# Kernel tuning notes

Hardware: AMD Instinct MI355X
Metric: run time of the kernel (lower is better)

## Reference

```python
import jax, jax.numpy as jnp
import numpy as np

EPS = 1e-6
CHUNK = 64
GATE_LOGIT_NORMALIZER = 16.0
NUM_HEADS = 4


def _rms(x, w):
    return x * jax.lax.rsqrt(jnp.mean(x * x, axis=-1, keepdims=True) + EPS) * w


def _gla_chunk(q, k, v, glog, num_heads):
    # q,k: [B,T,Dk] v: [B,T,Dv] glog: [B,T,Dk] (log decay, <=0)
    B, T, Dk = q.shape
    Dv = v.shape[-1]
    dk, dv = Dk // num_heads, Dv // num_heads
    Nc = T // CHUNK

    def split(x, d):
        # [B,T,H*d] -> [B,H,Nc,C,d]
        return x.reshape(B, T, num_heads, d).transpose(0, 2, 1, 3).reshape(B, num_heads, Nc, CHUNK, d)

    q, k, v, g = split(q, dk), split(k, dk), split(v, dv), split(glog, dk)
    b = jnp.cumsum(g, axis=3)  # inclusive cumulative log-decay within chunk
    scale = dk ** -0.5
    qe = q * jnp.exp(b) * scale

    # intra-chunk: A[t,s] = sum_d q_t k_s exp(b_t - b_s), causal (t>=s)
    mask = jnp.tril(jnp.ones((CHUNK, CHUNK), dtype=bool))
    A = jnp.einsum('bhncd,bhnsd->bhncs', qe, k * jnp.exp(-b))
    A = jnp.where(mask, A, 0.0)
    o_intra = jnp.einsum('bhncs,bhnsd->bhncd', A, v)

    # inter-chunk recurrence over state S: [B,H,dk,dv]
    def step(S, xs):
        qe_c, k_c, v_c, b_c = xs  # [B,H,C,*]
        blast = b_c[:, :, -1, :]                      # [B,H,dk]
        o_inter = jnp.einsum('bhcd,bhde->bhce', qe_c, S)
        kd = k_c * jnp.exp(blast[:, :, None, :] - b_c)
        S_new = S * jnp.exp(blast)[..., None] + jnp.einsum('bhcd,bhce->bhde', kd, v_c)
        return S_new, o_inter

    S0 = jnp.zeros((B, num_heads, dk, dv), q.dtype)
    xs = tuple(jnp.moveaxis(t, 2, 0) for t in (qe, k, v, b))
    _, o_inter = jax.lax.scan(step, S0, xs)
    o = o_intra + jnp.moveaxis(o_inter, 0, 2)  # [B,H,Nc,C,dv]
    return o.reshape(B, num_heads, T, dv).transpose(0, 2, 1, 3)  # [B,T,H,dv]


def setup_inputs() -> dict:
    key = jax.random.key(0)
    ks = jax.random.split(key, 12)
    B, T, Hs = 4, 2048, 1024
    Dk, Dv, I, R = 512, 1024, 2816, 16
    p = lambda k, s: jax.random.normal(k, s, jnp.float32) * 0.02
    return {
        'hidden_states': jax.random.normal(ks[0], (B, T, Hs), jnp.float32),
        'attn_norm_w': jnp.ones((Hs,), jnp.float32),
        'Wq': p(ks[1], (Hs, Dk)), 'Wk': p(ks[2], (Hs, Dk)), 'Wv': p(ks[3], (Hs, Dv)),
        'Wg': p(ks[4], (Hs, Dv)),
        'Wgk1': p(ks[5], (Hs, R)), 'Wgk2': p(ks[6], (R, Dk)), 'bgk2': jnp.zeros((Dk,), jnp.float32),
        'gnorm_w': jnp.ones((Dv // NUM_HEADS,), jnp.float32),
        'Wo': p(ks[7], (Dv, Hs)),
        'mlp_norm_w': jnp.ones((Hs,), jnp.float32),
        'W_gate': p(ks[8], (Hs, I)), 'W_up': p(ks[9], (Hs, I)), 'W_down': p(ks[10], (I, Hs)),
    }


def reference(hidden_states, attn_norm_w, Wq, Wk, Wv, Wg, Wgk1, Wgk2, bgk2,
              gnorm_w, Wo, mlp_norm_w, W_gate, W_up, W_down):
    x = hidden_states
    h = _rms(x, attn_norm_w)
    q, k, v = h @ Wq, h @ Wk, h @ Wv
    glog = jax.nn.log_sigmoid(h @ Wgk1 @ Wgk2 + bgk2) / GATE_LOGIT_NORMALIZER
    o = _gla_chunk(q, k, v, glog, NUM_HEADS)          # [B,T,H,dv]
    g_out = (h @ Wg).reshape(o.shape)
    o = _rms(o, gnorm_w) * (g_out * jax.nn.sigmoid(g_out))  # per-head RMSNorm + swish gate
    attn_out = o.reshape(x.shape[0], x.shape[1], -1) @ Wo
    # fused residual RMSNorm
    x2 = attn_out + x
    n = _rms(x2, mlp_norm_w)
    mlp = (jax.nn.silu(n @ W_gate) * (n @ W_up)) @ W_down
    return x2 + mlp
```

## Files before the change

### kernel.cpp

```cpp
#include <hip/hip_runtime.h>

typedef unsigned short u16;
typedef __attribute__((ext_vector_type(8))) short bf8_t;
typedef __attribute__((ext_vector_type(4))) float f4_t;

#define MFMA_B16(a,b,c) __builtin_amdgcn_mfma_f32_16x16x32_bf16(a,b,c,0,0,0)

__device__ __forceinline__ u16 f2bf(float f){
  union{ float f; unsigned u; } x; x.f = f;
  unsigned r = x.u + 0x7FFFu + ((x.u >> 16) & 1u);
  return (u16)(r >> 16);
}
__device__ __forceinline__ float bf2f(u16 u){
  union{ unsigned u; float f; } x; x.u = ((unsigned)u) << 16; return x.f;
}
__device__ __forceinline__ void gl_lds16(const void* g, void* l){
  __builtin_amdgcn_global_load_lds(
      (const __attribute__((address_space(1))) unsigned int*)g,
      (__attribute__((address_space(3))) unsigned int*)l, 16, 0, 0);
}
__device__ __forceinline__ int swz128(int row, int cb){ return row*128 + (cb ^ ((row & 7)  << 4)); }
__device__ __forceinline__ int swz256(int row, int cb){ return row*256 + (cb ^ ((row & 15) << 4)); }

__device__ __forceinline__ void xcd_map(int gx, int gy, int& bm, int& bn){
  const int i   = blockIdx.y*gx + blockIdx.x;
  const int cpx = (gx*gy) >> 3;
  const int j   = (i & 7)*cpx + (i >> 3);
  const int k   = j / (gx*8);
  const int jl  = j - k*(gx*8);
  bn = jl >> 3;
  bm = k*8 + (jl & 7);
}

#define TOKS 8192
#define HS   1024
#define DKTOT 512
#define DVTOT 1024
#define IM   2816

__global__ __launch_bounds__(256) void k_transpose(
    const float* __restrict__ W, u16* __restrict__ Wt, int K, int N)
{
  __shared__ float tile[64][65];
  const int n0 = blockIdx.x*64, k0 = blockIdx.y*64;
  const int tx = threadIdx.x & 63, tg = threadIdx.x >> 6;
  #pragma unroll
  for(int i=0;i<16;i++){
    int kr = tg*16 + i;
    tile[kr][tx] = W[(size_t)(k0+kr)*N + n0 + tx];
  }
  __syncthreads();
  #pragma unroll
  for(int i=0;i<16;i++){
    int nr = tg*16 + i;
    Wt[(size_t)(n0+nr)*K + k0 + tx] = f2bf(tile[tx][nr]);
  }
}

__global__ __launch_bounds__(256) void k_rmsnorm(
    const float* __restrict__ X, const float* __restrict__ W, u16* __restrict__ H)
{
  __shared__ float red[4];
  const size_t row = blockIdx.x;
  const int t = threadIdx.x;
  const float4 v = ((const float4*)(X + row*1024))[t];
  float ss = v.x*v.x + v.y*v.y + v.z*v.z + v.w*v.w;
  #pragma unroll
  for(int m=32;m>=1;m>>=1) ss += __shfl_xor(ss, m, 64);
  if((t & 63) == 0) red[t >> 6] = ss;
  __syncthreads();
  ss = red[0] + red[1] + red[2] + red[3];
  const float rs = rsqrtf(ss*(1.f/1024.f) + 1e-6f);
  const float4 w = ((const float4*)W)[t];
  ushort4 o;
  o.x = f2bf(v.x*rs*w.x);
  o.y = f2bf(v.y*rs*w.y);
  o.z = f2bf(v.z*rs*w.z);
  o.w = f2bf(v.w*rs*w.w);
  ((ushort4*)H)[row*256 + t] = o;
}

__global__ __launch_bounds__(256) void k_glog(
    const u16* __restrict__ H, const float* __restrict__ W1,
    const float* __restrict__ W2, const float* __restrict__ bias,
    float* __restrict__ G)
{
  __shared__ float hs[1024];
  __shared__ float red[16][17];
  __shared__ float rr[16];
  const size_t row = blockIdx.x;
  const int t = threadIdx.x;
  #pragma unroll
  for(int j=0;j<4;j++) hs[t*4+j] = bf2f(H[row*1024 + t*4 + j]);
  __syncthreads();
  const int r = t & 15, c = t >> 4;
  float acc = 0.f;
  #pragma unroll
  for(int j=0;j<64;j++){
    int k = c*64 + ((j + c) & 63);
    acc += hs[k] * W1[(size_t)k*16 + r];
  }
  red[c][r] = acc;
  __syncthreads();
  if(t < 16){
    float s2 = 0.f;
    #pragma unroll
    for(int cc=0;cc<16;cc++) s2 += red[cc][t];
    rr[t] = s2;
  }
  __syncthreads();
  #pragma unroll
  for(int dd=0;dd<2;dd++){
    int dcol = t + dd*256;
    float z = bias[dcol];
    #pragma unroll
    for(int j=0;j<16;j++) z += rr[j]*W2[j*512 + dcol];
    float ls = fminf(z, 0.f) - log1pf(__expf(-fabsf(z)));
    G[row*512 + dcol] = ls * 0.0625f;
  }
}

enum { E_BF16=1, E_ADDF32=2, E_SILUMUL=3, E_TRANS=4 };

template<int EPI>
__global__ __launch_bounds__(512, 2) void k_gemm8(
    const u16* __restrict__ A, const u16* __restrict__ Bt,
    void* __restrict__ Cp, const void* __restrict__ aux,
    int M, int N, int K)
{
  __shared__ __align__(16) u16 lds[3*24576];
  const int t = threadIdx.x;
  const int wv = t >> 6, ln = t & 63, lr = ln & 15, lg = ln >> 4;
  const int wm = wv >> 2, wn = wv & 3;
  int bm, bn; xcd_map(gridDim.x, gridDim.y, bm, bn);
  const int m0 = bm*128, n0 = bn*256;
  const int NT = K >> 6;

  const int sr = t >> 3;
  const int sc = ((t & 7)*16 ^ ((sr & 7) << 4)) >> 1;
  const u16* Asrc = A  + (size_t)(m0 + sr)*K + sc;
  const u16* Bsrc = Bt + (size_t)(n0 + sr)*K + sc;

  auto stage = [&](int T){
    const int b = T % 3;
    const size_t ko = (size_t)T * 64;
    u16* dA = lds + b*24576 + wv*512;
    u16* dB = lds + b*24576 + 8192 + wv*512;
    gl_lds16(Asrc + ko,                    dA);
    gl_lds16(Asrc + (size_t)64*K + ko,     dA + 4096);
    #pragma unroll
    for(int j=0;j<4;j++)
      gl_lds16(Bsrc + (size_t)(j*64)*K + ko, dB + j*4096);
  };

  f4_t acc[4][4];
  #pragma unroll
  for(int i=0;i<4;i++)
    #pragma unroll
    for(int j=0;j<4;j++) acc[i][j] = f4_t{0.f,0.f,0.f,0.f};

  const int rA = wm*64 + lr;
  const int rB = wn*64 + lr;
  const int cxor = (lr & 7) << 4;

  auto compute = [&](int b){
    const char* La = (const char*)(lds + b*24576);
    const char* Lb = La + 16384;
    #pragma unroll
    for(int kk=0;kk<2;++kk){
      const int cb = (kk*64 + lg*16) ^ cxor;
      bf8_t af[4], bfr[4];
      #pragma unroll
      for(int m=0;m<4;m++) af[m]  = *(const bf8_t*)(La + (rA + m*16)*128 + cb);
      #pragma unroll
      for(int n=0;n<4;n++) bfr[n] = *(const bf8_t*)(Lb + (rB + n*16)*128 + cb);
      __builtin_amdgcn_s_setprio(1);
      #pragma unroll
      for(int m=0;m<4;m++)
        #pragma unroll
        for(int n=0;n<4;n++)
          acc[m][n] = MFMA_B16(af[m], bfr[n], acc[m][n]);
      __builtin_amdgcn_s_setprio(0);
    }
  };

  stage(0);
  stage(1);

  for(int T=0; T<NT-1; ++T){
    asm volatile("s_waitcnt vmcnt(6)" ::: "memory");
    __builtin_amdgcn_s_barrier();
    asm volatile("" ::: "memory");
    __builtin_amdgcn_sched_barrier(0);
    if(T+2 < NT) stage(T+2);
    compute(T % 3);
  }
  asm volatile("s_waitcnt vmcnt(0)" ::: "memory");
  __builtin_amdgcn_s_barrier();
  asm volatile("" ::: "memory");
  __builtin_amdgcn_sched_barrier(0);
  compute((NT-1) % 3);

  #pragma unroll
  for(int m=0;m<4;m++){
    #pragma unroll
    for(int n=0;n<4;n++){
      const int row0 = m0 + wm*64 + m*16 + lg*4;
      const int col  = n0 + wn*64 + n*16 + lr;
      if constexpr(EPI==E_TRANS){
        ushort4 u;
        u.x = f2bf(acc[m][n][0]); u.y = f2bf(acc[m][n][1]);
        u.z = f2bf(acc[m][n][2]); u.w = f2bf(acc[m][n][3]);
        *(ushort4*)((u16*)Cp + (size_t)col*M + row0) = u;
      } else {
        #pragma unroll
        for(int r=0;r<4;r++){
          const size_t idx = (size_t)(row0+r)*N + col;
          float v = acc[m][n][r];
          if constexpr(EPI==E_BF16) ((u16*)Cp)[idx] = f2bf(v);
          else if constexpr(EPI==E_ADDF32) ((float*)Cp)[idx] = v + ((const float*)aux)[idx];
          else if constexpr(EPI==E_SILUMUL){
            float u = bf2f(((const u16*)aux)[idx]);
            ((u16*)Cp)[idx] = f2bf(u * v / (1.f + __expf(-v)));
          }
        }
      }
    }
  }
}

__global__ __launch_bounds__(256) void k_gla_a(
    const u16* __restrict__ QK,
    const u16* __restrict__ VT, const float* __restrict__ G,
    u16* __restrict__ QE, u16* __restrict__ OI,
    u16* __restrict__ CT, float* __restrict__ DEC)
{
  __shared__ __align__(16) u16 qe_s[64*128];
  __shared__ __align__(16) u16 ke_s[64*128];
  __shared__ __align__(16) u16 kd_s[128*64];
  __shared__ __align__(16) u16 a_s [64*64];

  const int bid = blockIdx.x;
  const int nc = bid & 31, hh = (bid >> 5) & 3, bb = bid >> 7;
  const int bh = bb*4 + hh;
  const int tok0 = bb*2048 + nc*64;
  const int t = threadIdx.x;
  const size_t cbase = (size_t)(bh*32 + nc);

  if(t < 128){
    const int d = t;
    const int col = hh*128 + d;
    float g[64];
    float blast = 0.f;
    #pragma unroll
    for(int i=0;i<64;i++){
      g[i] = G[(size_t)(tok0+i)*512 + col];
      blast += g[i];
    }
    DEC[cbase*128 + d] = __expf(blast);
    float cum = 0.f;
    #pragma unroll
    for(int i=0;i<64;i++){
      cum += g[i];
      float qv = bf2f(QK[(size_t)(tok0+i)*1024 + col]);
      float kv = bf2f(QK[(size_t)(tok0+i)*1024 + 512 + col]);
      float qe = qv * __expf(cum) * 0.08838834764831845f;
      float ke = kv * __expf(-cum);
      float kd = kv * __expf(blast - cum);
      *(u16*)((char*)qe_s + swz256(i, d*2)) = f2bf(qe);
      *(u16*)((char*)ke_s + swz256(i, d*2)) = f2bf(ke);
      *(u16*)((char*)kd_s + swz128(d, i*2)) = f2bf(kd);
      QE[(cbase*64 + i)*128 + d] = f2bf(qe);
    }
  }
  __syncthreads();

  const int wv = t >> 6, ln = t & 63, lr = ln & 15, lg = ln >> 4;

  bf8_t aq[4];
  #pragma unroll
  for(int ks=0;ks<4;ks++)
    aq[ks] = *(const bf8_t*)((const char*)qe_s + swz256(wv*16 + lr, ks*64 + lg*16));
  #pragma unroll
  for(int n=0;n<4;n++){
    f4_t accA = f4_t{0.f,0.f,0.f,0.f};
    #pragma unroll
    for(int ks=0;ks<4;ks++){
      bf8_t bk = *(const bf8_t*)((const char*)ke_s + swz256(n*16 + lr, ks*64 + lg*16));
      accA = MFMA_B16(aq[ks], bk, accA);
    }
    #pragma unroll
    for(int r=0;r<4;r++){
      int i = wv*16 + lg*4 + r;
      int s = n*16 + lr;
      float v = (s <= i) ? accA[r] : 0.f;
      *(u16*)((char*)a_s + swz128(i, s*2)) = f2bf(v);
    }
  }
  __syncthreads();

  bf8_t af[2], kf[2][2];
  #pragma unroll
  for(int ks=0;ks<2;ks++)
    af[ks] = *(const bf8_t*)((const char*)a_s + swz128(wv*16 + lr, ks*64 + lg*16));
  #pragma unroll
  for(int p=0;p<2;p++)
    #pragma unroll
    for(int ks=0;ks<2;ks++)
      kf[p][ks] = *(const bf8_t*)((const char*)kd_s + swz128((2*wv+p)*16 + lr, ks*64 + lg*16));

  #pragma unroll 4
  for(int ne=0; ne<16; ne++){
    bf8_t vf[2];
    #pragma unroll
    for(int ks=0;ks<2;ks++)
      vf[ks] = *(const bf8_t*)(VT + (size_t)(hh*256 + ne*16 + lr)*8192 + tok0 + ks*32 + lg*8);
    f4_t ao = f4_t{0.f,0.f,0.f,0.f};
    ao = MFMA_B16(af[0], vf[0], ao);
    ao = MFMA_B16(af[1], vf[1], ao);
    #pragma unroll
    for(int r=0;r<4;r++)
      OI[(cbase*64 + wv*16 + lg*4 + r)*256 + ne*16 + lr] = f2bf(ao[r]);
    f4_t c0 = f4_t{0.f,0.f,0.f,0.f}, c1 = f4_t{0.f,0.f,0.f,0.f};
    c0 = MFMA_B16(kf[0][0], vf[0], c0);
    c0 = MFMA_B16(kf[0][1], vf[1], c0);
    c1 = MFMA_B16(kf[1][0], vf[0], c1);
    c1 = MFMA_B16(kf[1][1], vf[1], c1);
    u16* dst = CT + (cbase*256 + ne*16 + lr)*128;
    ushort4 u0, u1;
    u0.x=f2bf(c0[0]); u0.y=f2bf(c0[1]); u0.z=f2bf(c0[2]); u0.w=f2bf(c0[3]);
    u1.x=f2bf(c1[0]); u1.y=f2bf(c1[1]); u1.z=f2bf(c1[2]); u1.w=f2bf(c1[3]);
    *(ushort4*)(dst + (2*wv+0)*16 + lg*4) = u0;
    *(ushort4*)(dst + (2*wv+1)*16 + lg*4) = u1;
  }
}

__global__ __launch_bounds__(256) void k_scan(
    u16* __restrict__ CTST, const float* __restrict__ DEC)
{
  const int idx = blockIdx.x*256 + threadIdx.x;
  const int d = idx & 127;
  const int e = (idx >> 7) & 255;
  const int bh = idx >> 15;
  float s = 0.f;
  for(int n=0;n<32;n++){
    const size_t off = ((size_t)(bh*32 + n)*256 + e)*128 + d;
    float c = bf2f(CTST[off]);
    CTST[off] = f2bf(s);
    s = s * DEC[(bh*32+n)*128 + d] + c;
  }
}

__global__ __launch_bounds__(256) void k_gla_c(
    const u16* __restrict__ QE, const u16* __restrict__ ST,
    const u16* __restrict__ OI, const u16* __restrict__ GO,
    const float* __restrict__ GW, u16* __restrict__ OG)
{
  const int bid = blockIdx.x;
  const int nc = bid & 31, hh = (bid >> 5) & 3, bb = bid >> 7;
  const int bh = bb*4 + hh;
  const int tok0 = bb*2048 + nc*64;
  const int t = threadIdx.x;
  const int wv = t >> 6, ln = t & 63, lr = ln & 15, lg = ln >> 4;
  const size_t cbase = (size_t)(bh*32 + nc);

  bf8_t qf[4];
  #pragma unroll
  for(int ks=0;ks<4;ks++)
    qf[ks] = *(const bf8_t*)(QE + (cbase*64 + wv*16 + lr)*128 + ks*32 + lg*8);

  f4_t acc[16];
  #pragma unroll
  for(int ne=0;ne<16;ne++){
    f4_t a = f4_t{0.f,0.f,0.f,0.f};
    #pragma unroll
    for(int ks=0;ks<4;ks++){
      bf8_t sf = *(const bf8_t*)(ST + (cbase*256 + ne*16 + lr)*128 + ks*32 + lg*8);
      a = MFMA_B16(qf[ks], sf, a);
    }
    acc[ne] = a;
  }

  float vals[16][4];
  float ss[4] = {0.f,0.f,0.f,0.f};
  #pragma unroll
  for(int ne=0;ne<16;ne++)
    #pragma unroll
    for(int r=0;r<4;r++){
      float v = acc[ne][r] + bf2f(OI[(cbase*64 + wv*16 + lg*4 + r)*256 + ne*16 + lr]);
      vals[ne][r] = v;
      ss[r] += v*v;
    }
  #pragma unroll
  for(int r=0;r<4;r++){
    ss[r] += __shfl_xor(ss[r], 1, 64);
    ss[r] += __shfl_xor(ss[r], 2, 64);
    ss[r] += __shfl_xor(ss[r], 4, 64);
    ss[r] += __shfl_xor(ss[r], 8, 64);
  }
  float rs[4];
  #pragma unroll
  for(int r=0;r<4;r++) rs[r] = rsqrtf(ss[r]*(1.f/256.f) + 1e-6f);

  #pragma unroll
  for(int ne=0;ne<16;ne++)
    #pragma unroll
    for(int r=0;r<4;r++){
      int i = wv*16 + lg*4 + r;
      int e = ne*16 + lr;
      const size_t idx = (size_t)(tok0+i)*1024 + hh*256 + e;
      float gg = bf2f(GO[idx]);
      float sg = gg / (1.f + __expf(-gg));
      OG[idx] = f2bf(vals[ne][r]*rs[r]*GW[e]*sg);
    }
}

constexpr size_t OFF_WQT    = 0;
constexpr size_t OFF_WKT    = OFF_WQT    + (size_t)DKTOT*HS*2;
constexpr size_t OFF_WVT    = OFF_WKT    + (size_t)DKTOT*HS*2;
constexpr size_t OFF_WGT    = OFF_WVT    + (size_t)DVTOT*HS*2;
constexpr size_t OFF_WOT    = OFF_WGT    + (size_t)DVTOT*HS*2;
constexpr size_t OFF_WGATET = OFF_WOT    + (size_t)HS*DVTOT*2;
constexpr size_t OFF_WUPT   = OFF_WGATET + (size_t)IM*HS*2;
constexpr size_t OFF_WDOWNT = OFF_WUPT   + (size_t)IM*HS*2;
constexpr size_t OFF_QE     = OFF_WDOWNT + (size_t)HS*IM*2;
constexpr size_t OFF_CTST   = OFF_QE     + (size_t)TOKS*DKTOT*2;
constexpr size_t OFF_DEC    = OFF_CTST   + (size_t)512*256*128*2;
constexpr size_t OFF_R1     = OFF_DEC    + (size_t)512*128*4;
constexpr size_t OFF_QKB    = OFF_R1;
constexpr size_t OFF_GLOG   = OFF_QKB    + (size_t)TOKS*1024*2;
constexpr size_t OFF_VT     = OFF_GLOG   + (size_t)TOKS*DKTOT*4;
constexpr size_t OFF_UP     = OFF_R1;
constexpr size_t OFF_R3     = OFF_R1 + 50331648;
constexpr size_t OFF_H      = OFF_R3;
constexpr size_t OFF_OI     = OFF_R3;
constexpr size_t OFF_N2     = OFF_R3;
constexpr size_t OFF_R4     = OFF_R3 + 16777216;
constexpr size_t OFF_GO     = OFF_R4;
constexpr size_t OFF_OG     = OFF_R4;
constexpr size_t WS_NEED    = OFF_R4 + 16777216;

extern "C" void kernel_launch(void* const* d_in, const int* in_sizes, int n_in,
                              void* d_out, int out_size, void* d_ws, size_t ws_size,
                              hipStream_t stream) {
  (void)in_sizes; (void)n_in; (void)out_size;
  if (ws_size < WS_NEED) return;

  const float* x       = (const float*)d_in[0];
  const float* attn_w  = (const float*)d_in[1];
  const float* Wq      = (const float*)d_in[2];
  const float* Wk      = (const float*)d_in[3];
  const float* Wv      = (const float*)d_in[4];
  const float* Wg      = (const float*)d_in[5];
  const float* Wgk1    = (const float*)d_in[6];
  const float* Wgk2    = (const float*)d_in[7];
  const float* bgk2    = (const float*)d_in[8];
  const float* gnw     = (const float*)d_in[9];
  const float* Wo      = (const float*)d_in[10];
  const float* mlpw    = (const float*)d_in[11];
  const float* Wgate   = (const float*)d_in[12];
  const float* Wup     = (const float*)d_in[13];
  const float* Wdown   = (const float*)d_in[14];
  char* ws = (char*)d_ws;

  u16*   wqt   = (u16*)(ws + OFF_WQT);
  u16*   wkt   = (u16*)(ws + OFF_WKT);
  u16*   wvt   = (u16*)(ws + OFF_WVT);
  u16*   wgt   = (u16*)(ws + OFF_WGT);
  u16*   wot   = (u16*)(ws + OFF_WOT);
  u16*   wgatet= (u16*)(ws + OFF_WGATET);
  u16*   wupt  = (u16*)(ws + OFF_WUPT);
  u16*   wdownt= (u16*)(ws + OFF_WDOWNT);
  u16*   qeb   = (u16*)(ws + OFF_QE);
  u16*   ctst  = (u16*)(ws + OFF_CTST);
  float* decb  = (float*)(ws + OFF_DEC);
  u16*   qkb   = (u16*)(ws + OFF_QKB);
  float* glogb = (float*)(ws + OFF_GLOG);
  u16*   vtb   = (u16*)(ws + OFF_VT);
  u16*   upb   = (u16*)(ws + OFF_UP);
  u16*   hb    = (u16*)(ws + OFF_H);
  u16*   oib   = (u16*)(ws + OFF_OI);
  u16*   n2b   = (u16*)(ws + OFF_N2);
  u16*   gob   = (u16*)(ws + OFF_GO);
  u16*   ogb   = (u16*)(ws + OFF_OG);
  float* x2b   = (float*)d_out;

  dim3 blk(256);
  dim3 blk8(512);

  k_transpose<<<dim3(DKTOT/64, HS/64), blk, 0, stream>>>(Wq, wqt, HS, DKTOT);
  k_transpose<<<dim3(DKTOT/64, HS/64), blk, 0, stream>>>(Wk, wkt, HS, DKTOT);
  k_transpose<<<dim3(DVTOT/64, HS/64), blk, 0, stream>>>(Wv, wvt, HS, DVTOT);
  k_transpose<<<dim3(DVTOT/64, HS/64), blk, 0, stream>>>(Wg, wgt, HS, DVTOT);
  k_transpose<<<dim3(HS/64, DVTOT/64), blk, 0, stream>>>(Wo, wot, DVTOT, HS);
  k_transpose<<<dim3(IM/64, HS/64), blk, 0, stream>>>(Wgate, wgatet, HS, IM);
  k_transpose<<<dim3(IM/64, HS/64), blk, 0, stream>>>(Wup, wupt, HS, IM);
  k_transpose<<<dim3(HS/64, IM/64), blk, 0, stream>>>(Wdown, wdownt, IM, HS);

  k_rmsnorm<<<TOKS, blk, 0, stream>>>(x, attn_w, hb);
  k_gemm8<E_BF16> <<<dim3(4, 64), blk8, 0, stream>>>(hb, wqt, qkb, nullptr, TOKS, 1024, HS);
  k_gemm8<E_TRANS><<<dim3(4, 64), blk8, 0, stream>>>(hb, wvt, vtb, nullptr, TOKS, DVTOT, HS);
  k_gemm8<E_BF16> <<<dim3(4, 64), blk8, 0, stream>>>(hb, wgt, gob, nullptr, TOKS, DVTOT, HS);
  k_glog<<<TOKS, blk, 0, stream>>>(hb, Wgk1, Wgk2, bgk2, glogb);

  k_gla_a<<<512, blk, 0, stream>>>(qkb, vtb, glogb, qeb, oib, ctst, decb);
  k_scan <<<2048, blk, 0, stream>>>(ctst, decb);
  k_gla_c<<<512, blk, 0, stream>>>(qeb, ctst, oib, gob, gnw, ogb);

  k_gemm8<E_ADDF32><<<dim3(4, 64), blk8, 0, stream>>>(ogb, wot, x2b, x, TOKS, HS, DVTOT);

  k_rmsnorm<<<TOKS, blk, 0, stream>>>(x2b, mlpw, n2b);
  k_gemm8<E_BF16>   <<<dim3(11, 64), blk8, 0, stream>>>(n2b, wupt,   upb, nullptr, TOKS, IM, HS);
  k_gemm8<E_SILUMUL><<<dim3(11, 64), blk8, 0, stream>>>(n2b, wgatet, upb, upb,     TOKS, IM, HS);
  k_gemm8<E_ADDF32> <<<dim3(4, 64),  blk8, 0, stream>>>(upb, wdownt, x2b, x2b,     TOKS, HS, IM);
}
```

Measured before the change: 438.6 us.

## Merge weight transposes, fuse QKV/G projections into one GEMM, split cumsum

Collapses the eight per-weight transpose launches into a single segmented kernel, and replaces the three separate projection GEMMs (QK, V-transposed, G) with one wide GEMM over a contiguous transposed-weight buffer, using a new epilogue that routes columns to the right destination. The GLA chunk-prep stage now uses all 256 threads, split into two token halves combined through shared-memory partial sums, instead of leaving half the block idle. These changes are meant to cut launch overhead and improve GPU fill for the small GEMMs. They depend on the weight buffers being laid out contiguously and on the new epilogue's routing being correct.

After: 418.4 us. -4.6%, faster.

```diff
diff --git a/kernel.cpp b/kernel.cpp
--- a/kernel.cpp
+++ b/kernel.cpp
@@ -5,415 +5,12 @@
 typedef __attribute__((ext_vector_type(4))) float f4_t;
 
 #define MFMA_B16(a,b,c) __builtin_amdgcn_mfma_f32_16x16x32_bf16(a,b,c,0,0,0)
-
-__device__ __forceinline__ u16 f2bf(float f){
-  union{ float f; unsigned u; } x; x.f = f;
-  unsigned r = x.u + 0x7FFFu + ((x.u >> 16) & 1u);
-  return (u16)(r >> 16);
-}
-__device__ __forceinline__ float bf2f(u16 u){
-  union{ unsigned u; float f; } x; x.u = ((unsigned)u) << 16; return x.f;
-}
-__device__ __forceinline__ void gl_lds16(const void* g, void* l){
-  __builtin_amdgcn_global_load_lds(
-      (const __attribute__((address_space(1))) unsigned int*)g,
-      (__attribute__((address_space(3))) unsigned int*)l, 16, 0, 0);
-}
-__device__ __forceinline__ int swz128(int row, int cb){ return row*128 + (cb ^ ((row & 7)  << 4)); }
-__device__ __forceinline__ int swz256(int row, int cb){ return row*256 + (cb ^ ((row & 15) << 4)); }
-
-__device__ __forceinline__ void xcd_map(int gx, int gy, int& bm, int& bn){
-  const int i   = blockIdx.y*gx + blockIdx.x;
-  const int cpx = (gx*gy) >> 3;
-  const int j   = (i & 7)*cpx + (i >> 3);
-  const int k   = j / (gx*8);
-  const int jl  = j - k*(gx*8);
-  bn = jl >> 3;
-  bm = k*8 + (jl & 7);
-}
 
 #define TOKS 8192
 #define HS   1024
 #define DKTOT 512
 #define DVTOT 1024
 #define IM   2816
-
-__global__ __launch_bounds__(256) void k_transpose(
-    const float* __restrict__ W, u16* __restrict__ Wt, int K, int N)
-{
-  __shared__ float tile[64][65];
-  const int n0 = blockIdx.x*64, k0 = blockIdx.y*64;
-  const int tx = threadIdx.x & 63, tg = threadIdx.x >> 6;
-  #pragma unroll
-  for(int i=0;i<16;i++){
-    int kr = tg*16 + i;
-    tile[kr][tx] = W[(size_t)(k0+kr)*N + n0 + tx];
-  }
-  __syncthreads();
-  #pragma unroll
-  for(int i=0;i<16;i++){
-    int nr = tg*16 + i;
-    Wt[(size_t)(n0+nr)*K + k0 + tx] = f2bf(tile[tx][nr]);
-  }
-}
-
-__global__ __launch_bounds__(256) void k_rmsnorm(
-    const float* __restrict__ X, const float* __restrict__ W, u16* __restrict__ H)
-{
-  __shared__ float red[4];
-  const size_t row = blockIdx.x;
-  const int t = threadIdx.x;
-  const float4 v = ((const float4*)(X + row*1024))[t];
-  float ss = v.x*v.x + v.y*v.y + v.z*v.z + v.w*v.w;
-  #pragma unroll
-  for(int m=32;m>=1;m>>=1) ss += __shfl_xor(ss, m, 64);
-  if((t & 63) == 0) red[t >> 6] = ss;
-  __syncthreads();
-  ss = red[0] + red[1] + red[2] + red[3];
-  const float rs = rsqrtf(ss*(1.f/1024.f) + 1e-6f);
-  const float4 w = ((const float4*)W)[t];
-  ushort4 o;
-  o.x = f2bf(v.x*rs*w.x);
-  o.y = f2bf(v.y*rs*w.y);
-  o.z = f2bf(v.z*rs*w.z);
-  o.w = f2bf(v.w*rs*w.w);
-  ((ushort4*)H)[row*256 + t] = o;
-}
-
-__global__ __launch_bounds__(256) void k_glog(
-    const u16* __restrict__ H, const float* __restrict__ W1,
-    const float* __restrict__ W2, const float* __restrict__ bias,
-    float* __restrict__ G)
-{
-  __shared__ float hs[1024];
-  __shared__ float red[16][17];
-  __shared__ float rr[16];
-  const size_t row = blockIdx.x;
-  const int t = threadIdx.x;
-  #pragma unroll
-  for(int j=0;j<4;j++) hs[t*4+j] = bf2f(H[row*1024 + t*4 + j]);
-  __syncthreads();
-  const int r = t & 15, c = t >> 4;
-  float acc = 0.f;
-  #pragma unroll
-  for(int j=0;j<64;j++){
-    int k = c*64 + ((j + c) & 63);
-    acc += hs[k] * W1[(size_t)k*16 + r];
-  }
-  red[c][r] = acc;
-  __syncthreads();
-  if(t < 16){
-    float s2 = 0.f;
-    #pragma unroll
-    for(int cc=0;cc<16;cc++) s2 += red[cc][t];
-    rr[t] = s2;
-  }
-  __syncthreads();
-  #pragma unroll
-  for(int dd=0;dd<2;dd++){
-    int dcol = t + dd*256;
-    float z = bias[dcol];
-    #pragma unroll
-    for(int j=0;j<16;j++) z += rr[j]*W2[j*512 + dcol];
-    float ls = fminf(z, 0.f) - log1pf(__expf(-fabsf(z)));
-    G[row*512 + dcol] = ls * 0.0625f;
-  }
-}
-
-enum { E_BF16=1, E_ADDF32=2, E_SILUMUL=3, E_TRANS=4 };
-
-template<int EPI>
-__global__ __launch_bounds__(512, 2) void k_gemm8(
-    const u16* __restrict__ A, const u16* __restrict__ Bt,
-    void* __restrict__ Cp, const void* __restrict__ aux,
-    int M, int N, int K)
-{
-  __shared__ __align__(16) u16 lds[3*24576];
-  const int t = threadIdx.x;
-  const int wv = t >> 6, ln = t & 63, lr = ln & 15, lg = ln >> 4;
-  const int wm = wv >> 2, wn = wv & 3;
-  int bm, bn; xcd_map(gridDim.x, gridDim.y, bm, bn);
-  const int m0 = bm*128, n0 = bn*256;
-  const int NT = K >> 6;
-
-  const int sr = t >> 3;
-  const int sc = ((t & 7)*16 ^ ((sr & 7) << 4)) >> 1;
-  const u16* Asrc = A  + (size_t)(m0 + sr)*K + sc;
-  const u16* Bsrc = Bt + (size_t)(n0 + sr)*K + sc;
-
-  auto stage = [&](int T){
-    const int b = T % 3;
-    const size_t ko = (size_t)T * 64;
-    u16* dA = lds + b*24576 + wv*512;
-    u16* dB = lds + b*24576 + 8192 + wv*512;
-    gl_lds16(Asrc + ko,                    dA);
-    gl_lds16(Asrc + (size_t)64*K + ko,     dA + 4096);
-    #pragma unroll
-    for(int j=0;j<4;j++)
-      gl_lds16(Bsrc + (size_t)(j*64)*K + ko, dB + j*4096);
-  };
-
-  f4_t acc[4][4];
-  #pragma unroll
-  for(int i=0;i<4;i++)
-    #pragma unroll
-    for(int j=0;j<4;j++) acc[i][j] = f4_t{0.f,0.f,0.f,0.f};
-
-  const int rA = wm*64 + lr;
-  const int rB = wn*64 + lr;
-  const int cxor = (lr & 7) << 4;
-
-  auto compute = [&](int b){
-    const char* La = (const char*)(lds + b*24576);
-    const char* Lb = La + 16384;
-    #pragma unroll
-    for(int kk=0;kk<2;++kk){
-      const int cb = (kk*64 + lg*16) ^ cxor;
-      bf8_t af[4], bfr[4];
-      #pragma unroll
-      for(int m=0;m<4;m++) af[m]  = *(const bf8_t*)(La + (rA + m*16)*128 + cb);
-      #pragma unroll
-      for(int n=0;n<4;n++) bfr[n] = *(const bf8_t*)(Lb + (rB + n*16)*128 + cb);
-      __builtin_amdgcn_s_setprio(1);
-      #pragma unroll
-      for(int m=0;m<4;m++)
-        #pragma unroll
-        for(int n=0;n<4;n++)
-          acc[m][n] = MFMA_B16(af[m], bfr[n], acc[m][n]);
-      __builtin_amdgcn_s_setprio(0);
-    }
-  };
-
-  stage(0);
-  stage(1);
-
-  for(int T=0; T<NT-1; ++T){
-    asm volatile("s_waitcnt vmcnt(6)" ::: "memory");
-    __builtin_amdgcn_s_barrier();
-    asm volatile("" ::: "memory");
-    __builtin_amdgcn_sched_barrier(0);
-    if(T+2 < NT) stage(T+2);
-    compute(T % 3);
-  }
-  asm volatile("s_waitcnt vmcnt(0)" ::: "memory");
-  __builtin_amdgcn_s_barrier();
-  asm volatile("" ::: "memory");
-  __builtin_amdgcn_sched_barrier(0);
-  compute((NT-1) % 3);
-
-  #pragma unroll
-  for(int m=0;m<4;m++){
-    #pragma unroll
-    for(int n=0;n<4;n++){
-      const int row0 = m0 + wm*64 + m*16 + lg*4;
-      const int col  = n0 + wn*64 + n*16 + lr;
-      if constexpr(EPI==E_TRANS){
-        ushort4 u;
-        u.x = f2bf(acc[m][n][0]); u.y = f2bf(acc[m][n][1]);
-        u.z = f2bf(acc[m][n][2]); u.w = f2bf(acc[m][n][3]);
-        *(ushort4*)((u16*)Cp + (size_t)col*M + row0) = u;
-      } else {
-        #pragma unroll
-        for(int r=0;r<4;r++){
-          const size_t idx = (size_t)(row0+r)*N + col;
-          float v = acc[m][n][r];
-          if constexpr(EPI==E_BF16) ((u16*)Cp)[idx] = f2bf(v);
-          else if constexpr(EPI==E_ADDF32) ((float*)Cp)[idx] = v + ((const float*)aux)[idx];
-          else if constexpr(EPI==E_SILUMUL){
-            float u = bf2f(((const u16*)aux)[idx]);
-            ((u16*)Cp)[idx] = f2bf(u * v / (1.f + __expf(-v)));
-          }
-        }
-      }
-    }
-  }
-}
-
-__global__ __launch_bounds__(256) void k_gla_a(
-    const u16* __restrict__ QK,
-    const u16* __restrict__ VT, const float* __restrict__ G,
-    u16* __restrict__ QE, u16* __restrict__ OI,
-    u16* __restrict__ CT, float* __restrict__ DEC)
-{
-  __shared__ __align__(16) u16 qe_s[64*128];
-  __shared__ __align__(16) u16 ke_s[64*128];
-  __shared__ __align__(16) u16 kd_s[128*64];
-  __shared__ __align__(16) u16 a_s [64*64];
-
-  const int bid = blockIdx.x;
-  const int nc = bid & 31, hh = (bid >> 5) & 3, bb = bid >> 7;
-  const int bh = bb*4 + hh;
-  const int tok0 = bb*2048 + nc*64;
-  const int t = threadIdx.x;
-  const size_t cbase = (size_t)(bh*32 + nc);
-
-  if(t < 128){
-    const int d = t;
-    const int col = hh*128 + d;
-    float g[64];
-    float blast = 0.f;
-    #pragma unroll
-    for(int i=0;i<64;i++){
-      g[i] = G[(size_t)(tok0+i)*512 + col];
-      blast += g[i];
-    }
-    DEC[cbase*128 + d] = __expf(blast);
-    float cum = 0.f;
-    #pragma unroll
-    for(int i=0;i<64;i++){
-      cum += g[i];
-      float qv = bf2f(QK[(size_t)(tok0+i)*1024 + col]);
-      float kv = bf2f(QK[(size_t)(tok0+i)*1024 + 512 + col]);
-      float qe = qv * __expf(cum) * 0.08838834764831845f;
-      float ke = kv * __expf(-cum);
-      float kd = kv * __expf(blast - cum);
-      *(u16*)((char*)qe_s + swz256(i, d*2)) = f2bf(qe);
-      *(u16*)((char*)ke_s + swz256(i, d*2)) = f2bf(ke);
-      *(u16*)((char*)kd_s + swz128(d, i*2)) = f2bf(kd);
-      QE[(cbase*64 + i)*128 + d] = f2bf(qe);
-    }
-  }
-  __syncthreads();
-
-  const int wv = t >> 6, ln = t & 63, lr = ln & 15, lg = ln >> 4;
-
-  bf8_t aq[4];
-  #pragma unroll
-  for(int ks=0;ks<4;ks++)
-    aq[ks] = *(const bf8_t*)((const char*)qe_s + swz256(wv*16 + lr, ks*64 + lg*16));
-  #pragma unroll
-  for(int n=0;n<4;n++){
-    f4_t accA = f4_t{0.f,0.f,0.f,0.f};
-    #pragma unroll
-    for(int ks=0;ks<4;ks++){
-      bf8_t bk = *(const bf8_t*)((const char*)ke_s + swz256(n*16 + lr, ks*64 + lg*16));
-      accA = MFMA_B16(aq[ks], bk, accA);
-    }
-    #pragma unroll
-    for(int r=0;r<4;r++){
-      int i = wv*16 + lg*4 + r;
-      int s = n*16 + lr;
-      float v = (s <= i) ? accA[r] : 0.f;
-      *(u16*)((char*)a_s + swz128(i, s*2)) = f2bf(v);
-    }
-  }
-  __syncthreads();
-
-  bf8_t af[2], kf[2][2];
-  #pragma unroll
-  for(int ks=0;ks<2;ks++)
-    af[ks] = *(const bf8_t*)((const char*)a_s + swz128(wv*16 + lr, ks*64 + lg*16));
-  #pragma unroll
-  for(int p=0;p<2;p++)
-    #pragma unroll
-    for(int ks=0;ks<2;ks++)
-      kf[p][ks] = *(const bf8_t*)((const char*)kd_s + swz128((2*wv+p)*16 + lr, ks*64 + lg*16));
-
-  #pragma unroll 4
-  for(int ne=0; ne<16; ne++){
-    bf8_t vf[2];
-    #pragma unroll
-    for(int ks=0;ks<2;ks++)
-      vf[ks] = *(const bf8_t*)(VT + (size_t)(hh*256 + ne*16 + lr)*8192 + tok0 + ks*32 + lg*8);
-    f4_t ao = f4_t{0.f,0.f,0.f,0.f};
-    ao = MFMA_B16(af[0], vf[0], ao);
-    ao = MFMA_B16(af[1], vf[1], ao);
-    #pragma unroll
-    for(int r=0;r<4;r++)
-      OI[(cbase*64 + wv*16 + lg*4 + r)*256 + ne*16 + lr] = f2bf(ao[r]);
-    f4_t c0 = f4_t{0.f,0.f,0.f,0.f}, c1 = f4_t{0.f,0.f,0.f,0.f};
-    c0 = MFMA_B16(kf[0][0], vf[0], c0);
-    c0 = MFMA_B16(kf[0][1], vf[1], c0);
-    c1 = MFMA_B16(kf[1][0], vf[0], c1);
-    c1 = MFMA_B16(kf[1][1], vf[1], c1);
-    u16* dst = CT + (cbase*256 + ne*16 + lr)*128;
-    ushort4 u0, u1;
-    u0.x=f2bf(c0[0]); u0.y=f2bf(c0[1]); u0.z=f2bf(c0[2]); u0.w=f2bf(c0[3]);
-    u1.x=f2bf(c1[0]); u1.y=f2bf(c1[1]); u1.z=f2bf(c1[2]); u1.w=f2bf(c1[3]);
-    *(ushort4*)(dst + (2*wv+0)*16 + lg*4) = u0;
-    *(ushort4*)(dst + (2*wv+1)*16 + lg*4) = u1;
-  }
-}
-
-__global__ __launch_bounds__(256) void k_scan(
-    u16* __restrict__ CTST, const float* __restrict__ DEC)
-{
-  const int idx = blockIdx.x*256 + threadIdx.x;
-  const int d = idx & 127;
-  const int e = (idx >> 7) & 255;
-  const int bh = idx >> 15;
-  float s = 0.f;
-  for(int n=0;n<32;n++){
-    const size_t off = ((size_t)(bh*32 + n)*256 + e)*128 + d;
-    float c = bf2f(CTST[off]);
-    CTST[off] = f2bf(s);
-    s = s * DEC[(bh*32+n)*128 + d] + c;
-  }
-}
-
-__global__ __launch_bounds__(256) void k_gla_c(
-    const u16* __restrict__ QE, const u16* __restrict__ ST,
-    const u16* __restrict__ OI, const u16* __restrict__ GO,
-    const float* __restrict__ GW, u16* __restrict__ OG)
-{
-  const int bid = blockIdx.x;
-  const int nc = bid & 31, hh = (bid >> 5) & 3, bb = bid >> 7;
-  const int bh = bb*4 + hh;
-  const int tok0 = bb*2048 + nc*64;
-  const int t = threadIdx.x;
-  const int wv = t >> 6, ln = t & 63, lr = ln & 15, lg = ln >> 4;
-  const size_t cbase = (size_t)(bh*32 + nc);
-
-  bf8_t qf[4];
-  #pragma unroll
-  for(int ks=0;ks<4;ks++)
-    qf[ks] = *(const bf8_t*)(QE + (cbase*64 + wv*16 + lr)*128 + ks*32 + lg*8);
-
-  f4_t acc[16];
-  #pragma unroll
-  for(int ne=0;ne<16;ne++){
-    f4_t a = f4_t{0.f,0.f,0.f,0.f};
-    #pragma unroll
-    for(int ks=0;ks<4;ks++){
-      bf8_t sf = *(const bf8_t*)(ST + (cbase*256 + ne*16 + lr)*128 + ks*32 + lg*8);
-      a = MFMA_B16(qf[ks], sf, a);
-    }
-    acc[ne] = a;
-  }
-
-  float vals[16][4];
-  float ss[4] = {0.f,0.f,0.f,0.f};
-  #pragma unroll
-  for(int ne=0;ne<16;ne++)
-    #pragma unroll
-    for(int r=0;r<4;r++){
-      float v = acc[ne][r] + bf2f(OI[(cbase*64 + wv*16 + lg*4 + r)*256 + ne*16 + lr]);
-      vals[ne][r] = v;
-      ss[r] += v*v;
-    }
-  #pragma unroll
-  for(int r=0;r<4;r++){
-    ss[r] += __shfl_xor(ss[r], 1, 64);
-    ss[r] += __shfl_xor(ss[r], 2, 64);
-    ss[r] += __shfl_xor(ss[r], 4, 64);
-    ss[r] += __shfl_xor(ss[r], 8, 64);
-  }
-  float rs[4];
-  #pragma unroll
-  for(int r=0;r<4;r++) rs[r] = rsqrtf(ss[r]*(1.f/256.f) + 1e-6f);
-
-  #pragma unroll
-  for(int ne=0;ne<16;ne++)
-    #pragma unroll
-    for(int r=0;r<4;r++){
-      int i = wv*16 + lg*4 + r;
-      int e = ne*16 + lr;
-      const size_t idx = (size_t)(tok0+i)*1024 + hh*256 + e;
-      float gg = bf2f(GO[idx]);
-      float sg = gg / (1.f + __expf(-gg));
-      OG[idx] = f2bf(vals[ne][r]*rs[r]*GW[e]*sg);
-    }
-}
 
 constexpr size_t OFF_WQT    = 0;
 constexpr size_t OFF_WKT    = OFF_WQT    + (size_t)DKTOT*HS*2;
@@ -440,6 +37,452 @@
 constexpr size_t OFF_OG     = OFF_R4;
 constexpr size_t WS_NEED    = OFF_R4 + 16777216;
 
+__device__ __forceinline__ u16 f2bf(float f){
+  union{ float f; unsigned u; } x; x.f = f;
+  unsigned r = x.u + 0x7FFFu + ((x.u >> 16) & 1u);
+  return (u16)(r >> 16);
+}
+__device__ __forceinline__ float bf2f(u16 u){
+  union{ unsigned u; float f; } x; x.u = ((unsigned)u) << 16; return x.f;
+}
+__device__ __forceinline__ void gl_lds16(const void* g, void* l){
+  __builtin_amdgcn_global_load_lds(
+      (const __attribute__((address_space(1))) unsigned int*)g,
+      (__attribute__((address_space(3))) unsigned int*)l, 16, 0, 0);
+}
+__device__ __forceinline__ int swz128(int row, int cb){ return row*128 + (cb ^ ((row & 7)  << 4)); }
+__device__ __forceinline__ int swz256(int row, int cb){ return row*256 + (cb ^ ((row & 15) << 4)); }
+
+__device__ __forceinline__ void xcd_map(int gx, int gy, int& bm, int& bn){
+  const int i   = blockIdx.y*gx + blockIdx.x;
+  const int cpx = (gx*gy) >> 3;
+  const int j   = (i & 7)*cpx + (i >> 3);
+  const int k   = j / (gx*8);
+  const int jl  = j - k*(gx*8);
+  bn = jl >> 3;
+  bm = k*8 + (jl & 7);
+}
+
+struct TransAll {
+  const float* src[8];
+  u16* dst[8];
+  int K[8];
+  int N[8];
+  int end[8];
+};
+
+__global__ __launch_bounds__(256) void k_transpose_all(TransAll ta)
+{
+  __shared__ float tile[64][65];
+  const int flat = blockIdx.x;
+  int seg = 0, start = 0;
+  #pragma unroll
+  for(int j=0;j<8;j++){
+    if(flat >= ta.end[j]){ seg = j+1; start = ta.end[j]; }
+  }
+  const float* W = ta.src[seg];
+  u16* Wt = ta.dst[seg];
+  const int K = ta.K[seg], N = ta.N[seg];
+  const int local = flat - start;
+  const int tilesX = N >> 6;
+  const int n0 = (local % tilesX)*64, k0 = (local / tilesX)*64;
+  const int tx = threadIdx.x & 63, tg = threadIdx.x >> 6;
+  #pragma unroll
+  for(int i=0;i<16;i++){
+    int kr = tg*16 + i;
+    tile[kr][tx] = W[(size_t)(k0+kr)*N + n0 + tx];
+  }
+  __syncthreads();
+  #pragma unroll
+  for(int i=0;i<16;i++){
+    int nr = tg*16 + i;
+    Wt[(size_t)(n0+nr)*K + k0 + tx] = f2bf(tile[tx][nr]);
+  }
+}
+
+__global__ __launch_bounds__(256) void k_rmsnorm(
+    const float* __restrict__ X, const float* __restrict__ W, u16* __restrict__ H)
+{
+  __shared__ float red[4];
+  const size_t row = blockIdx.x;
+  const int t = threadIdx.x;
+  const float4 v = ((const float4*)(X + row*1024))[t];
+  float ss = v.x*v.x + v.y*v.y + v.z*v.z + v.w*v.w;
+  #pragma unroll
+  for(int m=32;m>=1;m>>=1) ss += __shfl_xor(ss, m, 64);
+  if((t & 63) == 0) red[t >> 6] = ss;
+  __syncthreads();
+  ss = red[0] + red[1] + red[2] + red[3];
+  const float rs = rsqrtf(ss*(1.f/1024.f) + 1e-6f);
+  const float4 w = ((const float4*)W)[t];
+  ushort4 o;
+  o.x = f2bf(v.x*rs*w.x);
+  o.y = f2bf(v.y*rs*w.y);
+  o.z = f2bf(v.z*rs*w.z);
+  o.w = f2bf(v.w*rs*w.w);
+  ((ushort4*)H)[row*256 + t] = o;
+}
+
+__global__ __launch_bounds__(256) void k_glog(
+    const u16* __restrict__ H, const float* __restrict__ W1,
+    const float* __restrict__ W2, const float* __restrict__ bias,
+    float* __restrict__ G)
+{
+  __shared__ float hs[1024];
+  __shared__ float red[16][17];
+  __shared__ float rr[16];
+  const size_t row = blockIdx.x;
+  const int t = threadIdx.x;
+  #pragma unroll
+  for(int j=0;j<4;j++) hs[t*4+j] = bf2f(H[row*1024 + t*4 + j]);
+  __syncthreads();
+  const int r = t & 15, c = t >> 4;
+  float acc = 0.f;
+  #pragma unroll
+  for(int j=0;j<64;j++){
+    int k = c*64 + ((j + c) & 63);
+    acc += hs[k] * W1[(size_t)k*16 + r];
+  }
+  red[c][r] = acc;
+  __syncthreads();
+  if(t < 16){
+    float s2 = 0.f;
+    #pragma unroll
+    for(int cc=0;cc<16;cc++) s2 += red[cc][t];
+    rr[t] = s2;
+  }
+  __syncthreads();
+  #pragma unroll
+  for(int dd=0;dd<2;dd++){
+    int dcol = t + dd*256;
+    float z = bias[dcol];
+    #pragma unroll
+    for(int j=0;j<16;j++) z += rr[j]*W2[j*512 + dcol];
+    float ls = fminf(z, 0.f) - log1pf(__expf(-fabsf(z)));
+    G[row*512 + dcol] = ls * 0.0625f;
+  }
+}
+
+enum { E_BF16=1, E_ADDF32=2, E_SILUMUL=3, E_TRANS=4, E_QKVG=5 };
+
+template<int EPI>
+__global__ __launch_bounds__(512, 2) void k_gemm8(
+    const u16* __restrict__ A, const u16* __restrict__ Bt,
+    void* __restrict__ Cp, const void* __restrict__ aux,
+    int M, int N, int K)
+{
+  __shared__ __align__(16) u16 lds[3*24576];
+  const int t = threadIdx.x;
+  const int wv = t >> 6, ln = t & 63, lr = ln & 15, lg = ln >> 4;
+  const int wm = wv >> 2, wn = wv & 3;
+  int bm, bn; xcd_map(gridDim.x, gridDim.y, bm, bn);
+  const int m0 = bm*128, n0 = bn*256;
+  const int NT = K >> 6;
+
+  const int sr = t >> 3;
+  const int sc = ((t & 7)*16 ^ ((sr & 7) << 4)) >> 1;
+  const u16* Asrc = A  + (size_t)(m0 + sr)*K + sc;
+  const u16* Bsrc = Bt + (size_t)(n0 + sr)*K + sc;
+
+  auto stage = [&](int T){
+    const int b = T % 3;
+    const size_t ko = (size_t)T * 64;
+    u16* dA = lds + b*24576 + wv*512;
+    u16* dB = lds + b*24576 + 8192 + wv*512;
+    gl_lds16(Asrc + ko,                    dA);
+    gl_lds16(Asrc + (size_t)64*K + ko,     dA + 4096);
+    #pragma unroll
+    for(int j=0;j<4;j++)
+      gl_lds16(Bsrc + (size_t)(j*64)*K + ko, dB + j*4096);
+  };
+
+  f4_t acc[4][4];
+  #pragma unroll
+  for(int i=0;i<4;i++)
+    #pragma unroll
+    for(int j=0;j<4;j++) acc[i][j] = f4_t{0.f,0.f,0.f,0.f};
+
+  const int rA = wm*64 + lr;
+  const int rB = wn*64 + lr;
+  const int cxor = (lr & 7) << 4;
+
+  auto compute = [&](int b){
+    const char* La = (const char*)(lds + b*24576);
+    const char* Lb = La + 16384;
+    #pragma unroll
+    for(int kk=0;kk<2;++kk){
+      const int cb = (kk*64 + lg*16) ^ cxor;
+      bf8_t af[4], bfr[4];
+      #pragma unroll
+      for(int m=0;m<4;m++) af[m]  = *(const bf8_t*)(La + (rA + m*16)*128 + cb);
+      #pragma unroll
+      for(int n=0;n<4;n++) bfr[n] = *(const bf8_t*)(Lb + (rB + n*16)*128 + cb);
+      __builtin_amdgcn_s_setprio(1);
+      #pragma unroll
+      for(int m=0;m<4;m++)
+        #pragma unroll
+        for(int n=0;n<4;n++)
+          acc[m][n] = MFMA_B16(af[m], bfr[n], acc[m][n]);
+      __builtin_amdgcn_s_setprio(0);
+    }
+  };
+
+  stage(0);
+  stage(1);
+
+  for(int T=0; T<NT-1; ++T){
+    asm volatile("s_waitcnt vmcnt(6)" ::: "memory");
+    __builtin_amdgcn_s_barrier();
+    asm volatile("" ::: "memory");
+    __builtin_amdgcn_sched_barrier(0);
+    if(T+2 < NT) stage(T+2);
+    compute(T % 3);
+  }
+  asm volatile("s_waitcnt vmcnt(0)" ::: "memory");
+  __builtin_amdgcn_s_barrier();
+  asm volatile("" ::: "memory");
+  __builtin_amdgcn_sched_barrier(0);
+  compute((NT-1) % 3);
+
+  #pragma unroll
+  for(int m=0;m<4;m++){
+    #pragma unroll
+    for(int n=0;n<4;n++){
+      const int row0 = m0 + wm*64 + m*16 + lg*4;
+      const int col  = n0 + wn*64 + n*16 + lr;
+      if constexpr(EPI==E_TRANS){
+        ushort4 u;
+        u.x = f2bf(acc[m][n][0]); u.y = f2bf(acc[m][n][1]);
+        u.z = f2bf(acc[m][n][2]); u.w = f2bf(acc[m][n][3]);
+        *(ushort4*)((u16*)Cp + (size_t)col*M + row0) = u;
+      } else if constexpr(EPI==E_QKVG){
+        char* wsb = (char*)Cp;
+        if(n0 < 1024){
+          u16* dst = (u16*)(wsb + OFF_QKB);
+          #pragma unroll
+          for(int r=0;r<4;r++) dst[(size_t)(row0+r)*1024 + col] = f2bf(acc[m][n][r]);
+        } else if(n0 < 2048){
+          u16* dst = (u16*)(wsb + OFF_VT);
+          ushort4 u;
+          u.x = f2bf(acc[m][n][0]); u.y = f2bf(acc[m][n][1]);
+          u.z = f2bf(acc[m][n][2]); u.w = f2bf(acc[m][n][3]);
+          *(ushort4*)(dst + (size_t)(col-1024)*TOKS + row0) = u;
+        } else {
+          u16* dst = (u16*)(wsb + OFF_GO);
+          #pragma unroll
+          for(int r=0;r<4;r++) dst[(size_t)(row0+r)*1024 + (col-2048)] = f2bf(acc[m][n][r]);
+        }
+      } else {
+        #pragma unroll
+        for(int r=0;r<4;r++){
+          const size_t idx = (size_t)(row0+r)*N + col;
+          float v = acc[m][n][r];
+          if constexpr(EPI==E_BF16) ((u16*)Cp)[idx] = f2bf(v);
+          else if constexpr(EPI==E_ADDF32) ((float*)Cp)[idx] = v + ((const float*)aux)[idx];
+          else if constexpr(EPI==E_SILUMUL){
+            float u = bf2f(((const u16*)aux)[idx]);
+            ((u16*)Cp)[idx] = f2bf(u * v / (1.f + __expf(-v)));
+          }
+        }
+      }
+    }
+  }
+}
+
+__global__ __launch_bounds__(256) void k_gla_a(
+    const u16* __restrict__ QK,
+    const u16* __restrict__ VT, const float* __restrict__ G,
+    u16* __restrict__ QE, u16* __restrict__ OI,
+    u16* __restrict__ CT, float* __restrict__ DEC)
+{
+  __shared__ __align__(16) u16 qe_s[64*128];
+  __shared__ __align__(16) u16 ke_s[64*128];
+  __shared__ __align__(16) u16 kd_s[128*64];
+  __shared__ __align__(16) u16 a_s [64*64];
+  __shared__ float ps_s[2][128];
+
+  const int bid = blockIdx.x;
+  const int nc = bid & 31, hh = (bid >> 5) & 3, bb = bid >> 7;
+  const int bh = bb*4 + hh;
+  const int tok0 = bb*2048 + nc*64;
+  const int t = threadIdx.x;
+  const size_t cbase = (size_t)(bh*32 + nc);
+
+  {
+    const int d = t & 127;
+    const int half = t >> 7;
+    const int col = hh*128 + d;
+    const int i0 = half*32;
+    float g[32];
+    float psum = 0.f;
+    #pragma unroll
+    for(int i=0;i<32;i++){
+      g[i] = G[(size_t)(tok0+i0+i)*512 + col];
+      psum += g[i];
+    }
+    ps_s[half][d] = psum;
+    __syncthreads();
+    const float cum0  = half ? ps_s[0][d] : 0.f;
+    const float blast = ps_s[0][d] + ps_s[1][d];
+    if(half == 0) DEC[cbase*128 + d] = __expf(blast);
+    float cum = cum0;
+    #pragma unroll
+    for(int i=0;i<32;i++){
+      cum += g[i];
+      const int tok = tok0 + i0 + i;
+      float qv = bf2f(QK[(size_t)tok*1024 + col]);
+      float kv = bf2f(QK[(size_t)tok*1024 + 512 + col]);
+      float qe = qv * __expf(cum) * 0.08838834764831845f;
+      float ke = kv * __expf(-cum);
+      float kd = kv * __expf(blast - cum);
+      *(u16*)((char*)qe_s + swz256(i0+i, d*2)) = f2bf(qe);
+      *(u16*)((char*)ke_s + swz256(i0+i, d*2)) = f2bf(ke);
+      *(u16*)((char*)kd_s + swz128(d, (i0+i)*2)) = f2bf(kd);
+      QE[(cbase*64 + i0+i)*128 + d] = f2bf(qe);
+    }
+  }
+  __syncthreads();
+
+  const int wv = t >> 6, ln = t & 63, lr = ln & 15, lg = ln >> 4;
+
+  bf8_t aq[4];
+  #pragma unroll
+  for(int ks=0;ks<4;ks++)
+    aq[ks] = *(const bf8_t*)((const char*)qe_s + swz256(wv*16 + lr, ks*64 + lg*16));
+  #pragma unroll
+  for(int n=0;n<4;n++){
+    f4_t accA = f4_t{0.f,0.f,0.f,0.f};
+    #pragma unroll
+    for(int ks=0;ks<4;ks++){
+      bf8_t bk = *(const bf8_t*)((const char*)ke_s + swz256(n*16 + lr, ks*64 + lg*16));
+      accA = MFMA_B16(aq[ks], bk, accA);
+    }
+    #pragma unroll
+    for(int r=0;r<4;r++){
+      int i = wv*16 + lg*4 + r;
+      int s = n*16 + lr;
+      float v = (s <= i) ? accA[r] : 0.f;
+      *(u16*)((char*)a_s + swz128(i, s*2)) = f2bf(v);
+    }
+  }
+  __syncthreads();
+
+  bf8_t af[2], kf[2][2];
+  #pragma unroll
+  for(int ks=0;ks<2;ks++)
+    af[ks] = *(const bf8_t*)((const char*)a_s + swz128(wv*16 + lr, ks*64 + lg*16));
+  #pragma unroll
+  for(int p=0;p<2;p++)
+    #pragma unroll
+    for(int ks=0;ks<2;ks++)
+      kf[p][ks] = *(const bf8_t*)((const char*)kd_s + swz128((2*wv+p)*16 + lr, ks*64 + lg*16));
+
+  #pragma unroll 4
+  for(int ne=0; ne<16; ne++){
+    bf8_t vf[2];
+    #pragma unroll
+    for(int ks=0;ks<2;ks++)
+      vf[ks] = *(const bf8_t*)(VT + (size_t)(hh*256 + ne*16 + lr)*8192 + tok0 + ks*32 + lg*8);
+    f4_t ao = f4_t{0.f,0.f,0.f,0.f};
+    ao = MFMA_B16(af[0], vf[0], ao);
+    ao = MFMA_B16(af[1], vf[1], ao);
+    #pragma unroll
+    for(int r=0;r<4;r++)
+      OI[(cbase*64 + wv*16 + lg*4 + r)*256 + ne*16 + lr] = f2bf(ao[r]);
+    f4_t c0 = f4_t{0.f,0.f,0.f,0.f}, c1 = f4_t{0.f,0.f,0.f,0.f};
+    c0 = MFMA_B16(kf[0][0], vf[0], c0);
+    c0 = MFMA_B16(kf[0][1], vf[1], c0);
+    c1 = MFMA_B16(kf[1][0], vf[0], c1);
+    c1 = MFMA_B16(kf[1][1], vf[1], c1);
+    u16* dst = CT + (cbase*256 + ne*16 + lr)*128;
+    ushort4 u0, u1;
+    u0.x=f2bf(c0[0]); u0.y=f2bf(c0[1]); u0.z=f2bf(c0[2]); u0.w=f2bf(c0[3]);
+    u1.x=f2bf(c1[0]); u1.y=f2bf(c1[1]); u1.z=f2bf(c1[2]); u1.w=f2bf(c1[3]);
+    *(ushort4*)(dst + (2*wv+0)*16 + lg*4) = u0;
+    *(ushort4*)(dst + (2*wv+1)*16 + lg*4) = u1;
+  }
+}
+
+__global__ __launch_bounds__(256) void k_scan(
+    u16* __restrict__ CTST, const float* __restrict__ DEC)
+{
+  const int idx = blockIdx.x*256 + threadIdx.x;
+  const int d = idx & 127;
+  const int e = (idx >> 7) & 255;
+  const int bh = idx >> 15;
+  float s = 0.f;
+  for(int n=0;n<32;n++){
+    const size_t off = ((size_t)(bh*32 + n)*256 + e)*128 + d;
+    float c = bf2f(CTST[off]);
+    CTST[off] = f2bf(s);
+    s = s * DEC[(bh*32+n)*128 + d] + c;
+  }
+}
+
+__global__ __launch_bounds__(256) void k_gla_c(
+    const u16* __restrict__ QE, const u16* __restrict__ ST,
+    const u16* __restrict__ OI, const u16* __restrict__ GO,
+    const float* __restrict__ GW, u16* __restrict__ OG)
+{
+  const int bid = blockIdx.x;
+  const int nc = bid & 31, hh = (bid >> 5) & 3, bb = bid >> 7;
+  const int bh = bb*4 + hh;
+  const int tok0 = bb*2048 + nc*64;
+  const int t = threadIdx.x;
+  const int wv = t >> 6, ln = t & 63, lr = ln & 15, lg = ln >> 4;
+  const size_t cbase = (size_t)(bh*32 + nc);
+
+  bf8_t qf[4];
+  #pragma unroll
+  for(int ks=0;ks<4;ks++)
+    qf[ks] = *(const bf8_t*)(QE + (cbase*64 + wv*16 + lr)*128 + ks*32 + lg*8);
+
+  f4_t acc[16];
+  #pragma unroll
+  for(int ne=0;ne<16;ne++){
+    f4_t a = f4_t{0.f,0.f,0.f,0.f};
+    #pragma unroll
+    for(int ks=0;ks<4;ks++){
+      bf8_t sf = *(const bf8_t*)(ST + (cbase*256 + ne*16 + lr)*128 + ks*32 + lg*8);
+      a = MFMA_B16(qf[ks], sf, a);
+    }
+    acc[ne] = a;
+  }
+
+  float vals[16][4];
+  float ss[4] = {0.f,0.f,0.f,0.f};
+  #pragma unroll
+  for(int ne=0;ne<16;ne++)
+    #pragma unroll
+    for(int r=0;r<4;r++){
+      float v = acc[ne][r] + bf2f(OI[(cbase*64 + wv*16 + lg*4 + r)*256 + ne*16 + lr]);
+      vals[ne][r] = v;
+      ss[r] += v*v;
+    }
+  #pragma unroll
+  for(int r=0;r<4;r++){
+    ss[r] += __shfl_xor(ss[r], 1, 64);
+    ss[r] += __shfl_xor(ss[r], 2, 64);
+    ss[r] += __shfl_xor(ss[r], 4, 64);
+    ss[r] += __shfl_xor(ss[r], 8, 64);
+  }
+  float rs[4];
+  #pragma unroll
+  for(int r=0;r<4;r++) rs[r] = rsqrtf(ss[r]*(1.f/256.f) + 1e-6f);
+
+  #pragma unroll
+  for(int ne=0;ne<16;ne++)
+    #pragma unroll
+    for(int r=0;r<4;r++){
+      int i = wv*16 + lg*4 + r;
+      int e = ne*16 + lr;
+      const size_t idx = (size_t)(tok0+i)*1024 + hh*256 + e;
+      float gg = bf2f(GO[idx]);
+      float sg = gg / (1.f + __expf(-gg));
+      OG[idx] = f2bf(vals[ne][r]*rs[r]*GW[e]*sg);
+    }
+}
+
 extern "C" void kernel_launch(void* const* d_in, const int* in_sizes, int n_in,
                               void* d_out, int out_size, void* d_ws, size_t ws_size,
                               hipStream_t stream) {
@@ -488,19 +531,23 @@
   dim3 blk(256);
   dim3 blk8(512);
 
-  k_transpose<<<dim3(DKTOT/64, HS/64), blk, 0, stream>>>(Wq, wqt, HS, DKTOT);
-  k_transpose<<<dim3(DKTOT/64, HS/64), blk, 0, stream>>>(Wk, wkt, HS, DKTOT);
-  k_transpose<<<dim3(DVTOT/64, HS/64), blk, 0, stream>>>(Wv, wvt, HS, DVTOT);
-  k_transpose<<<dim3(DVTOT/64, HS/64), blk, 0, stream>>>(Wg, wgt, HS, DVTOT);
-  k_transpose<<<dim3(HS/64, DVTOT/64), blk, 0, stream>>>(Wo, wot, DVTOT, HS);
-  k_transpose<<<dim3(IM/64, HS/64), blk, 0, stream>>>(Wgate, wgatet, HS, IM);
-  k_transpose<<<dim3(IM/64, HS/64), blk, 0, stream>>>(Wup, wupt, HS, IM);
-  k_transpose<<<dim3(HS/64, IM/64), blk, 0, stream>>>(Wdown, wdownt, IM, HS);
+  TransAll ta;
+  ta.src[0]=Wq;    ta.dst[0]=wqt;    ta.K[0]=HS;  ta.N[0]=DKTOT;
+  ta.src[1]=Wk;    ta.dst[1]=wkt;    ta.K[1]=HS;  ta.N[1]=DKTOT;
+  ta.src[2]=Wv;    ta.dst[2]=wvt;    ta.K[2]=HS;  ta.N[2]=DVTOT;
+  ta.src[3]=Wg;    ta.dst[3]=wgt;    ta.K[3]=HS;  ta.N[3]=DVTOT;
+  ta.src[4]=Wo;    ta.dst[4]=wot;    ta.K[4]=DVTOT; ta.N[4]=HS;
+  ta.src[5]=Wgate; ta.dst[5]=wgatet; ta.K[5]=HS;  ta.N[5]=IM;
+  ta.src[6]=Wup;   ta.dst[6]=wupt;   ta.K[6]=HS;  ta.N[6]=IM;
+  ta.src[7]=Wdown; ta.dst[7]=wdownt; ta.K[7]=IM;  ta.N[7]=HS;
+  {
+    int cum = 0;
+    for(int j=0;j<8;j++){ cum += (ta.N[j]>>6)*(ta.K[j]>>6); ta.end[j] = cum; }
+  }
+  k_transpose_all<<<3136, blk, 0, stream>>>(ta);
 
   k_rmsnorm<<<TOKS, blk, 0, stream>>>(x, attn_w, hb);
-  k_gemm8<E_BF16> <<<dim3(4, 64), blk8, 0, stream>>>(hb, wqt, qkb, nullptr, TOKS, 1024, HS);
-  k_gemm8<E_TRANS><<<dim3(4, 64), blk8, 0, stream>>>(hb, wvt, vtb, nullptr, TOKS, DVTOT, HS);
-  k_gemm8<E_BF16> <<<dim3(4, 64), blk8, 0, stream>>>(hb, wgt, gob, nullptr, TOKS, DVTOT, HS);
+  k_gemm8<E_QKVG><<<dim3(12, 64), blk8, 0, stream>>>(hb, wqt, ws, nullptr, TOKS, 3072, HS);
   k_glog<<<TOKS, blk, 0, stream>>>(hb, Wgk1, Wgk2, bgk2, glogb);
 
   k_gla_a<<<512, blk, 0, stream>>>(qkb, vtb, glogb, qeb, oib, ctst, decb);
```
